# Kernel tuning notes

Measured on AMD Instinct MI355X. Metric: run time of the kernel, lower is better.

The kernel has to match this reference:

```python
import jax, jax.numpy as jnp
import numpy as np

B, IC2, N, K = 8, 128, 2048, 32   # x: [B, 2*in_channels, N, k]
C, G = 64, 8                       # out_channels, groups
CPG = C // G                       # channels per group
EPS_BN = 1e-5


def conv1x1(x, w, b=None):
    # 1x1 conv over [B, Cin, N, K] with weight [Cout, Cin]
    y = jnp.einsum('oc,bcnk->bonk', w, x)
    if b is not None:
        y = y + b[None, :, None, None]
    return y


def bn(x, g, beta, m, v):
    # inference-mode BatchNorm2d
    scale = g / jnp.sqrt(v + EPS_BN)
    return x * scale[None, :, None, None] + (beta - m * scale)[None, :, None, None]


def lrelu(x):
    return jax.nn.leaky_relu(x, 0.2)


def setup_inputs() -> dict:
    key = jax.random.key(0)
    ks = jax.random.split(key, 32)
    d = {}
    d['x'] = jax.random.normal(ks[0], (B, IC2, N, K), jnp.float32)
    d['rel_pos'] = jax.random.normal(ks[1], (B, 3, N, K), jnp.float32)
    # pos_net
    d['pos_w1'] = jax.random.normal(ks[2], (C, 3), jnp.float32) * 0.1
    d['pos_bn_g'] = jax.random.uniform(ks[3], (C,), jnp.float32, 0.5, 1.5)
    d['pos_bn_b'] = jax.random.normal(ks[4], (C,), jnp.float32) * 0.1
    d['pos_bn_m'] = jax.random.normal(ks[5], (C,), jnp.float32) * 0.1
    d['pos_bn_v'] = jax.random.uniform(ks[6], (C,), jnp.float32, 0.5, 1.5)
    d['pos_w2'] = jax.random.normal(ks[7], (C, C), jnp.float32) * 0.1
    d['pos_b2'] = jax.random.normal(ks[8], (C,), jnp.float32) * 0.1
    # pe_proj
    d['pe_w'] = jax.random.normal(ks[9], (G, C), jnp.float32) * 0.1
    d['pe_b'] = jax.random.normal(ks[10], (G,), jnp.float32) * 0.1
    # trans (Conv+BN+LeakyReLU)
    d['trans_w'] = jax.random.normal(ks[11], (C, IC2), jnp.float32) * 0.1
    d['trans_bn_g'] = jax.random.uniform(ks[12], (C,), jnp.float32, 0.5, 1.5)
    d['trans_bn_b'] = jax.random.normal(ks[13], (C,), jnp.float32) * 0.1
    d['trans_bn_m'] = jax.random.normal(ks[14], (C,), jnp.float32) * 0.1
    d['trans_bn_v'] = jax.random.uniform(ks[15], (C,), jnp.float32, 0.5, 1.5)
    # gate_net (hidden 16)
    d['gate_w1'] = jax.random.normal(ks[16], (16, IC2), jnp.float32) * 0.1
    d['gate_bn_g'] = jax.random.uniform(ks[17], (16,), jnp.float32, 0.5, 1.5)
    d['gate_bn_b'] = jax.random.normal(ks[18], (16,), jnp.float32) * 0.1
    d['gate_bn_m'] = jax.random.normal(ks[19], (16,), jnp.float32) * 0.1
    d['gate_bn_v'] = jax.random.uniform(ks[20], (16,), jnp.float32, 0.5, 1.5)
    d['gate_w2'] = jax.random.normal(ks[21], (1, 16), jnp.float32) * 0.1
    d['gate_b2'] = jnp.full((1,), 2.0, jnp.float32)  # init.constant_(bias, 2.0)
    # attn_net (hidden C//4 = 16)
    d['attn_w1'] = jax.random.normal(ks[22], (C // 4, IC2), jnp.float32) * 0.1
    d['attn_bn_g'] = jax.random.uniform(ks[23], (C // 4,), jnp.float32, 0.5, 1.5)
    d['attn_bn_b'] = jax.random.normal(ks[24], (C // 4,), jnp.float32) * 0.1
    d['attn_bn_m'] = jax.random.normal(ks[25], (C // 4,), jnp.float32) * 0.1
    d['attn_bn_v'] = jax.random.uniform(ks[26], (C // 4,), jnp.float32, 0.5, 1.5)
    d['attn_w2'] = jax.random.normal(ks[27], (G, C // 4), jnp.float32) * 0.1
    d['attn_b2'] = jax.random.normal(ks[28], (G,), jnp.float32) * 0.1
    return d


def reference(x, rel_pos, pos_w1, pos_bn_g, pos_bn_b, pos_bn_m, pos_bn_v, pos_w2, pos_b2,
              pe_w, pe_b, trans_w, trans_bn_g, trans_bn_b, trans_bn_m, trans_bn_v,
              gate_w1, gate_bn_g, gate_bn_b, gate_bn_m, gate_bn_v, gate_w2, gate_b2,
              attn_w1, attn_bn_g, attn_bn_b, attn_bn_m, attn_bn_v, attn_w2, attn_b2):
    # pos_net: conv -> BN -> LeakyReLU -> conv(bias)
    pos_enc = conv1x1(lrelu(bn(conv1x1(rel_pos, pos_w1), pos_bn_g, pos_bn_b, pos_bn_m, pos_bn_v)),
                      pos_w2, pos_b2)                                    # [B,C,N,K]
    # trans: conv -> BN -> LeakyReLU, plus positional encoding
    trans_feat = lrelu(bn(conv1x1(x, trans_w), trans_bn_g, trans_bn_b, trans_bn_m, trans_bn_v)) + pos_enc
    # gate_net (dropout=identity in eval): -> sigmoid gate [B,1,N,K]
    gate_h = lrelu(bn(conv1x1(x, gate_w1), gate_bn_g, gate_bn_b, gate_bn_m, gate_bn_v))
    gate_map = jax.nn.sigmoid(conv1x1(gate_h, gate_w2, gate_b2))
    # attn_net -> grouped logits [B,G,N,K]
    attn_h = lrelu(bn(conv1x1(x, attn_w1), attn_bn_g, attn_bn_b, attn_bn_m, attn_bn_v))
    attn_logits = conv1x1(attn_h, attn_w2, attn_b2)
    attn_logits = attn_logits + conv1x1(pos_enc, pe_w, pe_b)             # pe_proj
    attn_logits = attn_logits + jnp.log(gate_map + 1e-6)                 # full mode: log-combine gate
    attn_w = jax.nn.softmax(attn_logits, axis=-1)                        # softmax over neighbors k
    attn_w_exp = jnp.repeat(attn_w, CPG, axis=1)                         # repeat_interleave -> [B,C,N,K]
    out_attn = jnp.sum(trans_feat * attn_w_exp, axis=-1)                 # [B,C,N]
    out_max = jnp.max(trans_feat * gate_map, axis=-1)                    # [B,C,N]
    return out_attn + out_max
```

## Files before the change

kernel.cpp:

```cpp
#include <hip/hip_runtime.h>


typedef __attribute__((ext_vector_type(8))) short bf16x8;
typedef __attribute__((ext_vector_type(4))) float f32x4;

#define EPS_BN 1e-5f

__device__ __forceinline__ unsigned pk2(float a, float b){
  unsigned ua = __float_as_uint(a) + 0x8000u;
  unsigned ub = __float_as_uint(b) + 0x8000u;
  return __builtin_amdgcn_perm(ub, ua, 0x07060302);
}
__device__ __forceinline__ short f2bf(float a){
  unsigned u = __float_as_uint(a);
  u += 0x7FFFu + ((u >> 16) & 1u);
  return (short)(u >> 16);
}
__device__ __forceinline__ bf16x8 mk8(float4 a, float4 b){
  union { bf16x8 v; unsigned u[4]; } t;
  t.u[0] = pk2(a.x, a.y); t.u[1] = pk2(a.z, a.w);
  t.u[2] = pk2(b.x, b.y); t.u[3] = pk2(b.z, b.w);
  return t.v;
}
__device__ __forceinline__ float lrelu(float v){ return fmaxf(v, 0.2f*v); }

template<int N>
__device__ __forceinline__ float ror16(float x){
  return __int_as_float(__builtin_amdgcn_mov_dpp(__float_as_int(x), 0x120+N, 0xF, 0xF, false));
}
__device__ __forceinline__ float rsum16(float v){
  v += ror16<1>(v); v += ror16<2>(v); v += ror16<4>(v); v += ror16<8>(v); return v;
}
__device__ __forceinline__ float rmax16(float v){
  v = fmaxf(v, ror16<1>(v)); v = fmaxf(v, ror16<2>(v));
  v = fmaxf(v, ror16<4>(v)); v = fmaxf(v, ror16<8>(v)); return v;
}

#define MFMA16(a,b,c) __builtin_amdgcn_mfma_f32_16x16x32_bf16((a),(b),(c),0,0,0)

__global__ __launch_bounds__(256, 2)
void gsl_fused(const float* __restrict__ x,       const float* __restrict__ rel_pos,
               const float* __restrict__ pos_w1,  const float* __restrict__ pos_g,
               const float* __restrict__ pos_bb,  const float* __restrict__ pos_m,
               const float* __restrict__ pos_v,   const float* __restrict__ pos_w2,
               const float* __restrict__ pos_b2,  const float* __restrict__ pe_w,
               const float* __restrict__ pe_b,    const float* __restrict__ trans_w,
               const float* __restrict__ tr_g,    const float* __restrict__ tr_bb,
               const float* __restrict__ tr_m,    const float* __restrict__ tr_v,
               const float* __restrict__ gate_w1, const float* __restrict__ ga_g,
               const float* __restrict__ ga_bb,   const float* __restrict__ ga_m,
               const float* __restrict__ ga_v,    const float* __restrict__ gate_w2,
               const float* __restrict__ gate_b2, const float* __restrict__ attn_w1,
               const float* __restrict__ at_g,    const float* __restrict__ at_bb,
               const float* __restrict__ at_m,    const float* __restrict__ at_v,
               const float* __restrict__ attn_w2, const float* __restrict__ attn_b2,
               float* __restrict__ out)
{
  __shared__ __align__(16) char smem[73216];
  short* xbuf  = (short*)smem;
  short* wmain = (short*)(smem + 34816);
  short* wpos2 = (short*)(smem + 60928);
  float* trQ  = (float*)(smem + 71296);
  float* p1T  = (float*)(smem + 72320);
  float* gaT  = (float*)(smem + 72832);
  float* atT  = (float*)(smem + 72960);
  float* peBt = (float*)(smem + 73088);

  const int tid = threadIdx.x;
  const int wv  = tid >> 6;
  const int l   = tid & 63;
  const int l15 = l & 15, g4 = l >> 4;
  const int bid = blockIdx.x;
  const int b    = bid >> 6;
  const int nblk = (bid & 63) << 5;

  if (tid < 192){
    int r = tid >> 1, c0 = (tid & 1) * 64;
    const float* src = (r < 64) ? (trans_w + r*128)
                     : (r < 80) ? (gate_w1 + (r-64)*128)
                                : (attn_w1 + (r-80)*128);
    src += c0;
    short* dst = wmain + r*136 + c0;
    #pragma unroll
    for (int j = 0; j < 8; ++j)
      *(bf16x8*)(dst + 8*j) = mk8(*(const float4*)(src + 8*j), *(const float4*)(src + 8*j + 4));
  } else {
    int r = tid - 192;
    const float* src = pos_w2 + r*64;
    short* dst = wpos2 + r*72;
    #pragma unroll
    for (int j = 0; j < 8; ++j)
      *(bf16x8*)(dst + 8*j) = mk8(*(const float4*)(src + 8*j), *(const float4*)(src + 8*j + 4));
  }
  if (tid < 64){
    float s = tr_g[tid] * rsqrtf(tr_v[tid] + EPS_BN);
    *(float4*)(trQ + 4*tid) = make_float4(s, tr_bb[tid] - tr_m[tid]*s, pos_b2[tid], 0.f);
    float s2 = pos_g[tid] * rsqrtf(pos_v[tid] + EPS_BN);
    p1T[2*tid] = s2; p1T[2*tid+1] = pos_bb[tid] - pos_m[tid]*s2;
  } else if (tid < 80){
    int c = tid - 64;
    float s = ga_g[c] * rsqrtf(ga_v[c] + EPS_BN);
    gaT[2*c] = s; gaT[2*c+1] = ga_bb[c] - ga_m[c]*s;
  } else if (tid < 96){
    int c = tid - 80;
    float s = at_g[c] * rsqrtf(at_v[c] + EPS_BN);
    atT[2*c] = s; atT[2*c+1] = at_bb[c] - at_m[c]*s;
  } else if (tid < 112){
    int r2 = tid - 96;
    float v = 0.f;
    if (r2 < 8){
      v = pe_b[r2];
      for (int c = 0; c < 64; ++c) v += pe_w[r2*64 + c] * pos_b2[c];
    }
    peBt[r2] = v;
  }
  {
    int o = 2*tid, r = o >> 6, j = o & 63;
    float c0 = 0.f, c1 = 0.f;
    for (int c = 0; c < 64; ++c){
      float a = pe_w[r*64 + c];
      c0 += a * pos_w2[c*64 + j];
      c1 += a * pos_w2[c*64 + j + 1];
    }
    *(unsigned*)(wpos2 + (64 + r)*72 + j) = pk2(c0, c1);
  }

  uint2 pw1p[4];
  #pragma unroll
  for (int m2 = 0; m2 < 4; ++m2){
    uint2 t = make_uint2(0u, 0u);
    if (g4 == 0){
      const float* rp = pos_w1 + (16*m2 + l15)*3;
      t.x = pk2(rp[0], rp[1]);
      t.y = pk2(rp[2], 0.f);
    }
    pw1p[m2] = t;
  }
  bf16x8 gaf;
  {
    bf16x8 t = {0,0,0,0,0,0,0,0};
    #pragma unroll
    for (int j = 0; j < 8; ++j){
      int k = 8*g4 + j;
      float v2 = 0.f;
      if (l15 < 8)       { if (k >= 16) v2 = attn_w2[l15*16 + (k-16)]; }
      else if (l15 == 8) { if (k < 16)  v2 = gate_w2[k]; }
      t[j] = f2bf(v2);
    }
    gaf = t;
  }
  const float gb2v = gate_b2[0];

  __syncthreads();

  float lcr[4];
  #pragma unroll
  for (int r = 0; r < 4; ++r){
    int row = 4*g4 + r;
    lcr[r] = peBt[row] + ((row < 8) ? attn_b2[row] : 0.f);
  }

  const int col0 = 32*wv + l15, col1 = col0 + 16;
  const int lc0 = l15, lc1 = l15 + 16;
  const int lq = l & 7, ld = l >> 3;
  const int colb = 32*wv + 4*lq;
  char*  slice = smem + wv*8704;
  short* h1b   = (short*)slice;
  short* gab   = (short*)(slice + 4608);
  const float* xp0 = x + (((long)(b*128 + 8*ld)) << 16) + colb;
  const float* rpb = rel_pos + (((long)(3*b)) << 16);
  float* outb = out + (((long)(b*64)) << 11) + nblk + wv;

  f32x4 fa[8], fb[8];
  float rc[6] = {0.f,0.f,0.f,0.f,0.f,0.f};
  {
    const long sb0 = (long)nblk * 32;
    #pragma unroll
    for (int j = 0; j < 8; ++j) fa[j] = *(const f32x4*)(xp0 + sb0 + (((long)j) << 16));
    #pragma unroll
    for (int j = 0; j < 8; ++j) fb[j] = *(const f32x4*)(xp0 + sb0 + (((long)(64+j)) << 16));
    if (g4 == 0){
      long sg = sb0 + col0;
      rc[0] = rpb[sg];          rc[1] = rpb[sg + 65536];      rc[2] = rpb[sg + 131072];
      rc[3] = rpb[sg + 16];     rc[4] = rpb[sg + 65536 + 16]; rc[5] = rpb[sg + 131072 + 16];
    }
  }

  for (int it = 0; it < 8; ++it){
    const long sbase = (long)nblk*32 + 128*it;

    #pragma unroll
    for (int i2 = 0; i2 < 4; ++i2){
      union { bf16x8 v; unsigned u[4]; } ta, tb2;
      ta.u[0] = pk2(fa[0][i2], fa[1][i2]); ta.u[1] = pk2(fa[2][i2], fa[3][i2]);
      ta.u[2] = pk2(fa[4][i2], fa[5][i2]); ta.u[3] = pk2(fa[6][i2], fa[7][i2]);
      *(bf16x8*)(xbuf + (colb+i2)*136 + 8*ld) = ta.v;
      tb2.u[0] = pk2(fb[0][i2], fb[1][i2]); tb2.u[1] = pk2(fb[2][i2], fb[3][i2]);
      tb2.u[2] = pk2(fb[4][i2], fb[5][i2]); tb2.u[3] = pk2(fb[6][i2], fb[7][i2]);
      *(bf16x8*)(xbuf + (colb+i2)*136 + 64 + 8*ld) = tb2.v;
    }

    const long nsb = sbase + ((it < 7) ? 128 : 0);
    #pragma unroll
    for (int j = 0; j < 8; ++j) fa[j] = *(const f32x4*)(xp0 + nsb + (((long)j) << 16));

    f32x4 acc[6][2];
    #pragma unroll
    for (int m = 0; m < 6; ++m){
      f32x4 z = {0.f,0.f,0.f,0.f};
      acc[m][0] = z; acc[m][1] = z;
    }
    #pragma unroll
    for (int ks = 0; ks < 4; ++ks){
      bf16x8 b0 = *(const bf16x8*)(xbuf + col0*136 + 32*ks + 8*g4);
      bf16x8 b1 = *(const bf16x8*)(xbuf + col1*136 + 32*ks + 8*g4);
      #pragma unroll
      for (int m = 0; m < 6; ++m){
        bf16x8 af = *(const bf16x8*)(wmain + (16*m + l15)*136 + 32*ks + 8*g4);
        acc[m][0] = MFMA16(af, b0, acc[m][0]);
        acc[m][1] = MFMA16(af, b1, acc[m][1]);
      }
    }

    #pragma unroll
    for (int j = 0; j < 8; ++j) fb[j] = *(const f32x4*)(xp0 + nsb + (((long)(64+j)) << 16));

    {
      bf16x8 rf0 = {0,0,0,0,0,0,0,0}, rf1 = {0,0,0,0,0,0,0,0};
      if (g4 == 0){
        union { bf16x8 v; unsigned u[4]; } t0, t1;
        t0.u[0] = pk2(rc[0], rc[1]); t0.u[1] = pk2(rc[2], 0.f); t0.u[2] = 0u; t0.u[3] = 0u;
        t1.u[0] = pk2(rc[3], rc[4]); t1.u[1] = pk2(rc[5], 0.f); t1.u[2] = 0u; t1.u[3] = 0u;
        rf0 = t0.v; rf1 = t1.v;
      }
      #pragma unroll
      for (int m2 = 0; m2 < 4; ++m2){
        union { bf16x8 v; unsigned u[4]; } aw;
        aw.u[0] = pw1p[m2].x; aw.u[1] = pw1p[m2].y; aw.u[2] = 0u; aw.u[3] = 0u;
        f32x4 z = {0.f,0.f,0.f,0.f};
        f32x4 d0 = MFMA16(aw.v, rf0, z);
        f32x4 d1 = MFMA16(aw.v, rf1, z);
        int cb2 = 16*m2 + 4*g4;
        float2 t0 = *(const float2*)(p1T + 2*(cb2+0));
        float2 t1 = *(const float2*)(p1T + 2*(cb2+1));
        float2 t2 = *(const float2*)(p1T + 2*(cb2+2));
        float2 t3 = *(const float2*)(p1T + 2*(cb2+3));
        float h0 = lrelu(t0.x*d0[0]+t0.y), h1v = lrelu(t1.x*d0[1]+t1.y);
        float h2 = lrelu(t2.x*d0[2]+t2.y), h3 = lrelu(t3.x*d0[3]+t3.y);
        *(uint2*)(h1b + lc0*72 + cb2) = make_uint2(pk2(h0,h1v), pk2(h2,h3));
        h0 = lrelu(t0.x*d1[0]+t0.y); h1v = lrelu(t1.x*d1[1]+t1.y);
        h2 = lrelu(t2.x*d1[2]+t2.y); h3 = lrelu(t3.x*d1[3]+t3.y);
        *(uint2*)(h1b + lc1*72 + cb2) = make_uint2(pk2(h0,h1v), pk2(h2,h3));
      }
    }
    if (g4 == 0){
      long sg = nsb + col0;
      rc[0] = rpb[sg];          rc[1] = rpb[sg + 65536];      rc[2] = rpb[sg + 131072];
      rc[3] = rpb[sg + 16];     rc[4] = rpb[sg + 65536 + 16]; rc[5] = rpb[sg + 131072 + 16];
    }

    #pragma unroll
    for (int m = 0; m < 4; ++m)
      #pragma unroll
      for (int r = 0; r < 4; ++r){
        float4 tq = *(const float4*)(trQ + 4*(16*m + 4*g4 + r));
        acc[m][0][r] = lrelu(tq.x*acc[m][0][r] + tq.y) + tq.z;
        acc[m][1][r] = lrelu(tq.x*acc[m][1][r] + tq.y) + tq.z;
      }

    f32x4 pac4[2];
    {
      f32x4 z = {0.f,0.f,0.f,0.f};
      pac4[0] = z; pac4[1] = z;
    }
    #pragma unroll
    for (int ks = 0; ks < 2; ++ks){
      bf16x8 h0 = *(const bf16x8*)(h1b + lc0*72 + 32*ks + 8*g4);
      bf16x8 h1v = *(const bf16x8*)(h1b + lc1*72 + 32*ks + 8*g4);
      #pragma unroll
      for (int m2 = 0; m2 < 4; ++m2){
        bf16x8 af = *(const bf16x8*)(wpos2 + (16*m2 + l15)*72 + 32*ks + 8*g4);
        acc[m2][0] = MFMA16(af, h0, acc[m2][0]);
        acc[m2][1] = MFMA16(af, h1v, acc[m2][1]);
      }
      bf16x8 af4 = *(const bf16x8*)(wpos2 + (64 + l15)*72 + 32*ks + 8*g4);
      pac4[0] = MFMA16(af4, h0, pac4[0]);
      pac4[1] = MFMA16(af4, h1v, pac4[1]);
    }

    {
      int hc = 4*g4;
      float2 g0p = *(const float2*)(gaT + 2*(hc+0));
      float2 g1p = *(const float2*)(gaT + 2*(hc+1));
      float2 g2p = *(const float2*)(gaT + 2*(hc+2));
      float2 g3p = *(const float2*)(gaT + 2*(hc+3));
      float2 a0p = *(const float2*)(atT + 2*(hc+0));
      float2 a1p = *(const float2*)(atT + 2*(hc+1));
      float2 a2p = *(const float2*)(atT + 2*(hc+2));
      float2 a3p = *(const float2*)(atT + 2*(hc+3));
      #pragma unroll
      for (int ct = 0; ct < 2; ++ct){
        int lc = (ct == 0) ? lc0 : lc1;
        float q0 = lrelu(g0p.x*acc[4][ct][0] + g0p.y), q1 = lrelu(g1p.x*acc[4][ct][1] + g1p.y);
        float q2 = lrelu(g2p.x*acc[4][ct][2] + g2p.y), q3 = lrelu(g3p.x*acc[4][ct][3] + g3p.y);
        *(uint2*)(gab + lc*40 + hc) = make_uint2(pk2(q0,q1), pk2(q2,q3));
        float a0 = lrelu(a0p.x*acc[5][ct][0] + a0p.y), a1 = lrelu(a1p.x*acc[5][ct][1] + a1p.y);
        float a2 = lrelu(a2p.x*acc[5][ct][2] + a2p.y), a3 = lrelu(a3p.x*acc[5][ct][3] + a3p.y);
        *(uint2*)(gab + lc*40 + 16 + hc) = make_uint2(pk2(a0,a1), pk2(a2,a3));
      }
    }

    f32x4 gac0 = {0.f,0.f,0.f,0.f}, gac1 = gac0;
    {
      bf16x8 g0 = *(const bf16x8*)(gab + lc0*40 + 8*g4);
      bf16x8 g1 = *(const bf16x8*)(gab + lc1*40 + 8*g4);
      gac0 = MFMA16(gaf, g0, gac0);
      gac1 = MFMA16(gaf, g1, gac1);
    }

    float gv0 = __shfl(gac0[0], 32 + l15, 64);
    float gv1 = __shfl(gac1[0], 32 + l15, 64);
    float gm0 = 1.f/(1.f + __expf(-(gv0 + gb2v)));
    float gm1 = 1.f/(1.f + __expf(-(gv1 + gb2v)));
    float lg0 = __logf(gm0 + 1e-6f), lg1 = __logf(gm1 + 1e-6f);

    float wg0[4], wg1[4];
    #pragma unroll
    for (int r = 0; r < 4; ++r){
      float t0 = gac0[r] + pac4[0][r] + lcr[r] + lg0;
      float t1 = gac1[r] + pac4[1][r] + lcr[r] + lg1;
      float mx = rmax16(fmaxf(t0, t1));
      float e0 = __expf(t0 - mx), e1 = __expf(t1 - mx);
      float inv = 1.f / rsum16(e0 + e1);
      wg0[r] = e0 * inv; wg1[r] = e1 * inv;
    }
    float wf0[8], wf1[8];
    #pragma unroll
    for (int gg = 0; gg < 8; ++gg){
      int src = 16*(gg >> 2) + l15;
      wf0[gg] = __shfl(wg0[gg & 3], src, 64);
      wf1[gg] = __shfl(wg1[gg & 3], src, 64);
    }
    const bool hi = (g4 >= 2);
    #pragma unroll
    for (int m = 0; m < 4; ++m){
      float w0 = hi ? wf0[2*m+1] : wf0[2*m];
      float w1 = hi ? wf1[2*m+1] : wf1[2*m];
      #pragma unroll
      for (int r = 0; r < 4; ++r){
        float sA = rsum16(acc[m][0][r]*w0 + acc[m][1][r]*w1);
        float sM = rmax16(fmaxf(acc[m][0][r]*gm0, acc[m][1][r]*gm1));
        if (l15 == 0)
          outb[(((long)(16*m + 4*g4 + r)) << 11) + 4*it] = sA + sM;
      }
    }
  }
}

extern "C" void kernel_launch(void* const* d_in, const int* in_sizes, int n_in,
                              void* d_out, int out_size, void* d_ws, size_t ws_size,
                              hipStream_t stream){
  (void)in_sizes; (void)n_in; (void)out_size; (void)d_ws; (void)ws_size;
  gsl_fused<<<dim3(512), dim3(256), 0, stream>>>(
    (const float*)d_in[0],  (const float*)d_in[1],  (const float*)d_in[2],
    (const float*)d_in[3],  (const float*)d_in[4],  (const float*)d_in[5],
    (const float*)d_in[6],  (const float*)d_in[7],  (const float*)d_in[8],
    (const float*)d_in[9],  (const float*)d_in[10], (const float*)d_in[11],
    (const float*)d_in[12], (const float*)d_in[13], (const float*)d_in[14],
    (const float*)d_in[15], (const float*)d_in[16], (const float*)d_in[17],
    (const float*)d_in[18], (const float*)d_in[19], (const float*)d_in[20],
    (const float*)d_in[21], (const float*)d_in[22], (const float*)d_in[23],
    (const float*)d_in[24], (const float*)d_in[25], (const float*)d_in[26],
    (const float*)d_in[27], (const float*)d_in[28], (const float*)d_in[29],
    (float*)d_out);
}
```

Baseline: 75.63 us.

## Load x directly into MFMA fragments, drop LDS staging, split prep kernel

Each lane now loads x straight from global memory in the layout the MFMA B-operand needs and converts it to bf16 in registers. This removes the shared-memory x staging buffer, its write/read traffic and the associated bank pressure. The pe_w·pos_w2 fold and the pe bias are moved into a separate one-block prep kernel that writes to the workspace, which removes per-block redundant work. LDS shrinks and row padding changes, the grid doubles to 1024 blocks of 16 points each, and launch bounds target 3 blocks per SM. In exchange, the scalar strided global loads are less coalesced, register pressure rises, and there is an extra kernel launch.

```diff
diff --git a/kernel.cpp b/kernel.cpp
--- a/kernel.cpp
+++ b/kernel.cpp
@@ -16,13 +16,18 @@
   u += 0x7FFFu + ((u >> 16) & 1u);
   return (short)(u >> 16);
 }
-__device__ __forceinline__ bf16x8 mk8(float4 a, float4 b){
-  union { bf16x8 v; unsigned u[4]; } t;
-  t.u[0] = pk2(a.x, a.y); t.u[1] = pk2(a.z, a.w);
-  t.u[2] = pk2(b.x, b.y); t.u[3] = pk2(b.z, b.w);
-  return t.v;
-}
 __device__ __forceinline__ float lrelu(float v){ return fmaxf(v, 0.2f*v); }
+
+__device__ __forceinline__ void st8(short* dst, float4 a, float4 b){
+  *(uint2*)(dst)     = make_uint2(pk2(a.x,a.y), pk2(a.z,a.w));
+  *(uint2*)(dst + 4) = make_uint2(pk2(b.x,b.y), pk2(b.z,b.w));
+}
+__device__ __forceinline__ bf16x8 ld8(const short* p){
+  union { bf16x8 v; uint2 q[2]; } w;
+  w.q[0] = *(const uint2*)(p);
+  w.q[1] = *(const uint2*)(p + 4);
+  return w.v;
+}
 
 template<int N>
 __device__ __forceinline__ float ror16(float x){
@@ -38,13 +43,49 @@
 
 #define MFMA16(a,b,c) __builtin_amdgcn_mfma_f32_16x16x32_bf16((a),(b),(c),0,0,0)
 
-__global__ __launch_bounds__(256, 2)
+__device__ __forceinline__ void loadfrag(float (&t)[32], const float* xc, long sg){
+  #pragma unroll
+  for (int ks = 0; ks < 4; ++ks)
+    #pragma unroll
+    for (int j = 0; j < 8; ++j)
+      t[ks*8+j] = xc[(((long)(32*ks + j)) << 16) + sg];
+}
+__device__ __forceinline__ void cvtfrag(bf16x8 (&xb)[4], const float (&t)[32]){
+  #pragma unroll
+  for (int ks = 0; ks < 4; ++ks){
+    union { bf16x8 v; unsigned u[4]; } w;
+    w.u[0] = pk2(t[8*ks+0], t[8*ks+1]);
+    w.u[1] = pk2(t[8*ks+2], t[8*ks+3]);
+    w.u[2] = pk2(t[8*ks+4], t[8*ks+5]);
+    w.u[3] = pk2(t[8*ks+6], t[8*ks+7]);
+    xb[ks] = w.v;
+  }
+}
+
+__global__ void gsl_prep(const float* __restrict__ pos_w2, const float* __restrict__ pe_w,
+                         const float* __restrict__ pe_b,   const float* __restrict__ pos_b2,
+                         float* __restrict__ ws){
+  int t = threadIdx.x;
+  int r = t >> 6, j = t & 63;
+  float s = 0.f;
+  for (int c = 0; c < 64; ++c) s += pe_w[r*64 + c] * pos_w2[c*64 + j];
+  ws[t] = s;
+  if (t < 16){
+    float v = 0.f;
+    if (t < 8){
+      v = pe_b[t];
+      for (int c = 0; c < 64; ++c) v += pe_w[t*64 + c] * pos_b2[c];
+    }
+    ws[512 + t] = v;
+  }
+}
+
+__global__ __launch_bounds__(256, 3)
 void gsl_fused(const float* __restrict__ x,       const float* __restrict__ rel_pos,
                const float* __restrict__ pos_w1,  const float* __restrict__ pos_g,
                const float* __restrict__ pos_bb,  const float* __restrict__ pos_m,
                const float* __restrict__ pos_v,   const float* __restrict__ pos_w2,
-               const float* __restrict__ pos_b2,  const float* __restrict__ pe_w,
-               const float* __restrict__ pe_b,    const float* __restrict__ trans_w,
+               const float* __restrict__ pos_b2,  const float* __restrict__ trans_w,
                const float* __restrict__ tr_g,    const float* __restrict__ tr_bb,
                const float* __restrict__ tr_m,    const float* __restrict__ tr_v,
                const float* __restrict__ gate_w1, const float* __restrict__ ga_g,
@@ -54,25 +95,45 @@
                const float* __restrict__ at_g,    const float* __restrict__ at_bb,
                const float* __restrict__ at_m,    const float* __restrict__ at_v,
                const float* __restrict__ attn_w2, const float* __restrict__ attn_b2,
-               float* __restrict__ out)
+               const float* __restrict__ ws,      float* __restrict__ out)
 {
-  __shared__ __align__(16) char smem[73216];
-  short* xbuf  = (short*)smem;
-  short* wmain = (short*)(smem + 34816);
-  short* wpos2 = (short*)(smem + 60928);
-  float* trQ  = (float*)(smem + 71296);
-  float* p1T  = (float*)(smem + 72320);
-  float* gaT  = (float*)(smem + 72832);
-  float* atT  = (float*)(smem + 72960);
-  float* peBt = (float*)(smem + 73088);
+  __shared__ __align__(16) char smem[54080];
+  short* wmain = (short*)smem;
+  short* wpos2 = (short*)(smem + 25344);
+  float* trT  = (float*)(smem + 52544);
+  float* pb2T = (float*)(smem + 53056);
+  float* p1T  = (float*)(smem + 53312);
+  float* gaT  = (float*)(smem + 53824);
+  float* atT  = (float*)(smem + 53952);
 
   const int tid = threadIdx.x;
   const int wv  = tid >> 6;
   const int l   = tid & 63;
   const int l15 = l & 15, g4 = l >> 4;
   const int bid = blockIdx.x;
-  const int b    = bid >> 6;
-  const int nblk = (bid & 63) << 5;
+  const int b    = bid >> 7;
+  const int nblk = (bid & 127) << 4;
+
+  const int col0 = 32*wv + l15, col1 = col0 + 16;
+  const int lc0 = l15, lc1 = l15 + 16;
+  const float* xcg = x + (((long)(b*128 + 8*g4)) << 16);
+  const float* rpb = rel_pos + (((long)(3*b)) << 16);
+  float* outb = out + (((long)(b*64)) << 11) + nblk + wv;
+  short* h1b = (short*)(smem + 35136 + wv*4352);
+  short* gab = h1b;
+
+  float t0[32], t1[32];
+  float rc[6] = {0.f,0.f,0.f,0.f,0.f,0.f};
+  {
+    const long sb0 = (long)nblk * 32;
+    loadfrag(t0, xcg, sb0 + col0);
+    loadfrag(t1, xcg, sb0 + col0 + 16);
+    if (g4 == 0){
+      long sg = sb0 + col0;
+      rc[0] = rpb[sg];          rc[1] = rpb[sg + 65536];      rc[2] = rpb[sg + 131072];
+      rc[3] = rpb[sg + 16];     rc[4] = rpb[sg + 65536 + 16]; rc[5] = rpb[sg + 131072 + 16];
+    }
+  }
 
   if (tid < 192){
     int r = tid >> 1, c0 = (tid & 1) * 64;
@@ -80,21 +141,30 @@
                      : (r < 80) ? (gate_w1 + (r-64)*128)
                                 : (attn_w1 + (r-80)*128);
     src += c0;
-    short* dst = wmain + r*136 + c0;
+    short* dst = wmain + r*132 + c0;
     #pragma unroll
     for (int j = 0; j < 8; ++j)
-      *(bf16x8*)(dst + 8*j) = mk8(*(const float4*)(src + 8*j), *(const float4*)(src + 8*j + 4));
+      st8(dst + 8*j, *(const float4*)(src + 8*j), *(const float4*)(src + 8*j + 4));
   } else {
     int r = tid - 192;
     const float* src = pos_w2 + r*64;
-    short* dst = wpos2 + r*72;
+    short* dst = wpos2 + r*68;
     #pragma unroll
     for (int j = 0; j < 8; ++j)
-      *(bf16x8*)(dst + 8*j) = mk8(*(const float4*)(src + 8*j), *(const float4*)(src + 8*j + 4));
+      st8(dst + 8*j, *(const float4*)(src + 8*j), *(const float4*)(src + 8*j + 4));
+  }
+  if (tid < 16){
+    int r = tid >> 1, c0 = (tid & 1) * 32;
+    const float* src = ws + r*64 + c0;
+    short* dst = wpos2 + (64 + r)*68 + c0;
+    #pragma unroll
+    for (int j = 0; j < 4; ++j)
+      st8(dst + 8*j, *(const float4*)(src + 8*j), *(const float4*)(src + 8*j + 4));
   }
   if (tid < 64){
     float s = tr_g[tid] * rsqrtf(tr_v[tid] + EPS_BN);
-    *(float4*)(trQ + 4*tid) = make_float4(s, tr_bb[tid] - tr_m[tid]*s, pos_b2[tid], 0.f);
+    trT[2*tid] = s; trT[2*tid+1] = tr_bb[tid] - tr_m[tid]*s;
+    pb2T[tid] = pos_b2[tid];
     float s2 = pos_g[tid] * rsqrtf(pos_v[tid] + EPS_BN);
     p1T[2*tid] = s2; p1T[2*tid+1] = pos_bb[tid] - pos_m[tid]*s2;
   } else if (tid < 80){
@@ -105,24 +175,6 @@
     int c = tid - 80;
     float s = at_g[c] * rsqrtf(at_v[c] + EPS_BN);
     atT[2*c] = s; atT[2*c+1] = at_bb[c] - at_m[c]*s;
-  } else if (tid < 112){
-    int r2 = tid - 96;
-    float v = 0.f;
-    if (r2 < 8){
-      v = pe_b[r2];
-      for (int c = 0; c < 64; ++c) v += pe_w[r2*64 + c] * pos_b2[c];
-    }
-    peBt[r2] = v;
-  }
-  {
-    int o = 2*tid, r = o >> 6, j = o & 63;
-    float c0 = 0.f, c1 = 0.f;
-    for (int c = 0; c < 64; ++c){
-      float a = pe_w[r*64 + c];
-      c0 += a * pos_w2[c*64 + j];
-      c1 += a * pos_w2[c*64 + j + 1];
-    }
-    *(unsigned*)(wpos2 + (64 + r)*72 + j) = pk2(c0, c1);
   }
 
   uint2 pw1p[4];
@@ -150,59 +202,22 @@
     gaf = t;
   }
   const float gb2v = gate_b2[0];
-
-  __syncthreads();
-
   float lcr[4];
   #pragma unroll
   for (int r = 0; r < 4; ++r){
     int row = 4*g4 + r;
-    lcr[r] = peBt[row] + ((row < 8) ? attn_b2[row] : 0.f);
-  }
-
-  const int col0 = 32*wv + l15, col1 = col0 + 16;
-  const int lc0 = l15, lc1 = l15 + 16;
-  const int lq = l & 7, ld = l >> 3;
-  const int colb = 32*wv + 4*lq;
-  char*  slice = smem + wv*8704;
-  short* h1b   = (short*)slice;
-  short* gab   = (short*)(slice + 4608);
-  const float* xp0 = x + (((long)(b*128 + 8*ld)) << 16) + colb;
-  const float* rpb = rel_pos + (((long)(3*b)) << 16);
-  float* outb = out + (((long)(b*64)) << 11) + nblk + wv;
-
-  f32x4 fa[8], fb[8];
-  float rc[6] = {0.f,0.f,0.f,0.f,0.f,0.f};
-  {
-    const long sb0 = (long)nblk * 32;
-    #pragma unroll
-    for (int j = 0; j < 8; ++j) fa[j] = *(const f32x4*)(xp0 + sb0 + (((long)j) << 16));
-    #pragma unroll
-    for (int j = 0; j < 8; ++j) fb[j] = *(const f32x4*)(xp0 + sb0 + (((long)(64+j)) << 16));
-    if (g4 == 0){
-      long sg = sb0 + col0;
-      rc[0] = rpb[sg];          rc[1] = rpb[sg + 65536];      rc[2] = rpb[sg + 131072];
-      rc[3] = rpb[sg + 16];     rc[4] = rpb[sg + 65536 + 16]; rc[5] = rpb[sg + 131072 + 16];
-    }
-  }
-
-  for (int it = 0; it < 8; ++it){
+    lcr[r] = ws[512 + row] + ((row < 8) ? attn_b2[row] : 0.f);
+  }
+
+  bf16x8 xb0[4], xb1[4];
+  cvtfrag(xb0, t0);
+  cvtfrag(xb1, t1);
+
+  __syncthreads();
+
+  for (int it = 0; it < 4; ++it){
     const long sbase = (long)nblk*32 + 128*it;
-
-    #pragma unroll
-    for (int i2 = 0; i2 < 4; ++i2){
-      union { bf16x8 v; unsigned u[4]; } ta, tb2;
-      ta.u[0] = pk2(fa[0][i2], fa[1][i2]); ta.u[1] = pk2(fa[2][i2], fa[3][i2]);
-      ta.u[2] = pk2(fa[4][i2], fa[5][i2]); ta.u[3] = pk2(fa[6][i2], fa[7][i2]);
-      *(bf16x8*)(xbuf + (colb+i2)*136 + 8*ld) = ta.v;
-      tb2.u[0] = pk2(fb[0][i2], fb[1][i2]); tb2.u[1] = pk2(fb[2][i2], fb[3][i2]);
-      tb2.u[2] = pk2(fb[4][i2], fb[5][i2]); tb2.u[3] = pk2(fb[6][i2], fb[7][i2]);
-      *(bf16x8*)(xbuf + (colb+i2)*136 + 64 + 8*ld) = tb2.v;
-    }
-
-    const long nsb = sbase + ((it < 7) ? 128 : 0);
-    #pragma unroll
-    for (int j = 0; j < 8; ++j) fa[j] = *(const f32x4*)(xp0 + nsb + (((long)j) << 16));
+    const long nsb = sbase + ((it < 3) ? 128 : 0);
 
     f32x4 acc[6][2];
     #pragma unroll
@@ -212,26 +227,23 @@
     }
     #pragma unroll
     for (int ks = 0; ks < 4; ++ks){
-      bf16x8 b0 = *(const bf16x8*)(xbuf + col0*136 + 32*ks + 8*g4);
-      bf16x8 b1 = *(const bf16x8*)(xbuf + col1*136 + 32*ks + 8*g4);
       #pragma unroll
       for (int m = 0; m < 6; ++m){
-        bf16x8 af = *(const bf16x8*)(wmain + (16*m + l15)*136 + 32*ks + 8*g4);
-        acc[m][0] = MFMA16(af, b0, acc[m][0]);
-        acc[m][1] = MFMA16(af, b1, acc[m][1]);
-      }
-    }
-
-    #pragma unroll
-    for (int j = 0; j < 8; ++j) fb[j] = *(const f32x4*)(xp0 + nsb + (((long)(64+j)) << 16));
+        bf16x8 af = ld8(wmain + (16*m + l15)*132 + 32*ks + 8*g4);
+        acc[m][0] = MFMA16(af, xb0[ks], acc[m][0]);
+        acc[m][1] = MFMA16(af, xb1[ks], acc[m][1]);
+      }
+    }
+
+    loadfrag(t0, xcg, nsb + col0);
 
     {
       bf16x8 rf0 = {0,0,0,0,0,0,0,0}, rf1 = {0,0,0,0,0,0,0,0};
       if (g4 == 0){
-        union { bf16x8 v; unsigned u[4]; } t0, t1;
-        t0.u[0] = pk2(rc[0], rc[1]); t0.u[1] = pk2(rc[2], 0.f); t0.u[2] = 0u; t0.u[3] = 0u;
-        t1.u[0] = pk2(rc[3], rc[4]); t1.u[1] = pk2(rc[5], 0.f); t1.u[2] = 0u; t1.u[3] = 0u;
-        rf0 = t0.v; rf1 = t1.v;
+        union { bf16x8 v; unsigned u[4]; } q0, q1;
+        q0.u[0] = pk2(rc[0], rc[1]); q0.u[1] = pk2(rc[2], 0.f); q0.u[2] = 0u; q0.u[3] = 0u;
+        q1.u[0] = pk2(rc[3], rc[4]); q1.u[1] = pk2(rc[5], 0.f); q1.u[2] = 0u; q1.u[3] = 0u;
+        rf0 = q0.v; rf1 = q1.v;
       }
       #pragma unroll
       for (int m2 = 0; m2 < 4; ++m2){
@@ -241,16 +253,16 @@
         f32x4 d0 = MFMA16(aw.v, rf0, z);
         f32x4 d1 = MFMA16(aw.v, rf1, z);
         int cb2 = 16*m2 + 4*g4;
-        float2 t0 = *(const float2*)(p1T + 2*(cb2+0));
-        float2 t1 = *(const float2*)(p1T + 2*(cb2+1));
-        float2 t2 = *(const float2*)(p1T + 2*(cb2+2));
-        float2 t3 = *(const float2*)(p1T + 2*(cb2+3));
-        float h0 = lrelu(t0.x*d0[0]+t0.y), h1v = lrelu(t1.x*d0[1]+t1.y);
-        float h2 = lrelu(t2.x*d0[2]+t2.y), h3 = lrelu(t3.x*d0[3]+t3.y);
-        *(uint2*)(h1b + lc0*72 + cb2) = make_uint2(pk2(h0,h1v), pk2(h2,h3));
-        h0 = lrelu(t0.x*d1[0]+t0.y); h1v = lrelu(t1.x*d1[1]+t1.y);
-        h2 = lrelu(t2.x*d1[2]+t2.y); h3 = lrelu(t3.x*d1[3]+t3.y);
-        *(uint2*)(h1b + lc1*72 + cb2) = make_uint2(pk2(h0,h1v), pk2(h2,h3));
+        float2 q0 = *(const float2*)(p1T + 2*(cb2+0));
+        float2 q1 = *(const float2*)(p1T + 2*(cb2+1));
+        float2 q2 = *(const float2*)(p1T + 2*(cb2+2));
+        float2 q3 = *(const float2*)(p1T + 2*(cb2+3));
+        float h0 = lrelu(q0.x*d0[0]+q0.y), h1v = lrelu(q1.x*d0[1]+q1.y);
+        float h2 = lrelu(q2.x*d0[2]+q2.y), h3 = lrelu(q3.x*d0[3]+q3.y);
+        *(uint2*)(h1b + lc0*68 + cb2) = make_uint2(pk2(h0,h1v), pk2(h2,h3));
+        h0 = lrelu(q0.x*d1[0]+q0.y); h1v = lrelu(q1.x*d1[1]+q1.y);
+        h2 = lrelu(q2.x*d1[2]+q2.y); h3 = lrelu(q3.x*d1[3]+q3.y);
+        *(uint2*)(h1b + lc1*68 + cb2) = make_uint2(pk2(h0,h1v), pk2(h2,h3));
       }
     }
     if (g4 == 0){
@@ -260,13 +272,18 @@
     }
 
     #pragma unroll
-    for (int m = 0; m < 4; ++m)
-      #pragma unroll
-      for (int r = 0; r < 4; ++r){
-        float4 tq = *(const float4*)(trQ + 4*(16*m + 4*g4 + r));
-        acc[m][0][r] = lrelu(tq.x*acc[m][0][r] + tq.y) + tq.z;
-        acc[m][1][r] = lrelu(tq.x*acc[m][1][r] + tq.y) + tq.z;
-      }
+    for (int m = 0; m < 4; ++m){
+      float4 tb01 = *(const float4*)(trT + 2*(16*m + 4*g4));
+      float4 tb23 = *(const float4*)(trT + 2*(16*m + 4*g4) + 4);
+      float4 pz   = *(const float4*)(pb2T + 16*m + 4*g4);
+      #pragma unroll
+      for (int ct = 0; ct < 2; ++ct){
+        acc[m][ct][0] = lrelu(tb01.x*acc[m][ct][0] + tb01.y) + pz.x;
+        acc[m][ct][1] = lrelu(tb01.z*acc[m][ct][1] + tb01.w) + pz.y;
+        acc[m][ct][2] = lrelu(tb23.x*acc[m][ct][2] + tb23.y) + pz.z;
+        acc[m][ct][3] = lrelu(tb23.z*acc[m][ct][3] + tb23.w) + pz.w;
+      }
+    }
 
     f32x4 pac4[2];
     {
@@ -275,18 +292,21 @@
     }
     #pragma unroll
     for (int ks = 0; ks < 2; ++ks){
-      bf16x8 h0 = *(const bf16x8*)(h1b + lc0*72 + 32*ks + 8*g4);
-      bf16x8 h1v = *(const bf16x8*)(h1b + lc1*72 + 32*ks + 8*g4);
+      bf16x8 h0 = ld8(h1b + lc0*68 + 32*ks + 8*g4);
+      bf16x8 h1v = ld8(h1b + lc1*68 + 32*ks + 8*g4);
       #pragma unroll
       for (int m2 = 0; m2 < 4; ++m2){
-        bf16x8 af = *(const bf16x8*)(wpos2 + (16*m2 + l15)*72 + 32*ks + 8*g4);
+        bf16x8 af = ld8(wpos2 + (16*m2 + l15)*68 + 32*ks + 8*g4);
         acc[m2][0] = MFMA16(af, h0, acc[m2][0]);
         acc[m2][1] = MFMA16(af, h1v, acc[m2][1]);
       }
-      bf16x8 af4 = *(const bf16x8*)(wpos2 + (64 + l15)*72 + 32*ks + 8*g4);
+      bf16x8 af4 = ld8(wpos2 + (64 + l15)*68 + 32*ks + 8*g4);
       pac4[0] = MFMA16(af4, h0, pac4[0]);
       pac4[1] = MFMA16(af4, h1v, pac4[1]);
     }
+
+    cvtfrag(xb0, t0);
+    loadfrag(t1, xcg, nsb + col0 + 16);
 
     {
       int hc = 4*g4;
@@ -327,25 +347,23 @@
     float wg0[4], wg1[4];
     #pragma unroll
     for (int r = 0; r < 4; ++r){
-      float t0 = gac0[r] + pac4[0][r] + lcr[r] + lg0;
-      float t1 = gac1[r] + pac4[1][r] + lcr[r] + lg1;
-      float mx = rmax16(fmaxf(t0, t1));
-      float e0 = __expf(t0 - mx), e1 = __expf(t1 - mx);
+      float tt0 = gac0[r] + pac4[0][r] + lcr[r] + lg0;
+      float tt1 = gac1[r] + pac4[1][r] + lcr[r] + lg1;
+      float mx = rmax16(fmaxf(tt0, tt1));
+      float e0 = __expf(tt0 - mx), e1 = __expf(tt1 - mx);
       float inv = 1.f / rsum16(e0 + e1);
       wg0[r] = e0 * inv; wg1[r] = e1 * inv;
     }
-    float wf0[8], wf1[8];
-    #pragma unroll
-    for (int gg = 0; gg < 8; ++gg){
-      int src = 16*(gg >> 2) + l15;
-      wf0[gg] = __shfl(wg0[gg & 3], src, 64);
-      wf1[gg] = __shfl(wg1[gg & 3], src, 64);
-    }
     const bool hi = (g4 >= 2);
     #pragma unroll
     for (int m = 0; m < 4; ++m){
-      float w0 = hi ? wf0[2*m+1] : wf0[2*m];
-      float w1 = hi ? wf1[2*m+1] : wf1[2*m];
+      int src = 16*(m >> 1) + l15;
+      float a0 = __shfl(wg0[(2*m) & 3], src, 64);
+      float b0 = __shfl(wg0[(2*m+1) & 3], src, 64);
+      float a1 = __shfl(wg1[(2*m) & 3], src, 64);
+      float b1 = __shfl(wg1[(2*m+1) & 3], src, 64);
+      float w0 = hi ? b0 : a0;
+      float w1 = hi ? b1 : a1;
       #pragma unroll
       for (int r = 0; r < 4; ++r){
         float sA = rsum16(acc[m][0][r]*w0 + acc[m][1][r]*w1);
@@ -354,23 +372,27 @@
           outb[(((long)(16*m + 4*g4 + r)) << 11) + 4*it] = sA + sM;
       }
     }
+
+    cvtfrag(xb1, t1);
   }
 }
 
 extern "C" void kernel_launch(void* const* d_in, const int* in_sizes, int n_in,
                               void* d_out, int out_size, void* d_ws, size_t ws_size,
                               hipStream_t stream){
-  (void)in_sizes; (void)n_in; (void)out_size; (void)d_ws; (void)ws_size;
-  gsl_fused<<<dim3(512), dim3(256), 0, stream>>>(
+  (void)in_sizes; (void)n_in; (void)out_size; (void)ws_size;
+  gsl_prep<<<dim3(1), dim3(512), 0, stream>>>(
+    (const float*)d_in[7], (const float*)d_in[9], (const float*)d_in[10],
+    (const float*)d_in[8], (float*)d_ws);
+  gsl_fused<<<dim3(1024), dim3(256), 0, stream>>>(
     (const float*)d_in[0],  (const float*)d_in[1],  (const float*)d_in[2],
     (const float*)d_in[3],  (const float*)d_in[4],  (const float*)d_in[5],
     (const float*)d_in[6],  (const float*)d_in[7],  (const float*)d_in[8],
-    (const float*)d_in[9],  (const float*)d_in[10], (const float*)d_in[11],
-    (const float*)d_in[12], (const float*)d_in[13], (const float*)d_in[14],
-    (const float*)d_in[15], (const float*)d_in[16], (const float*)d_in[17],
-    (const float*)d_in[18], (const float*)d_in[19], (const float*)d_in[20],
-    (const float*)d_in[21], (const float*)d_in[22], (const float*)d_in[23],
-    (const float*)d_in[24], (const float*)d_in[25], (const float*)d_in[26],
-    (const float*)d_in[27], (const float*)d_in[28], (const float*)d_in[29],
-    (float*)d_out);
-}
+    (const float*)d_in[11], (const float*)d_in[12], (const float*)d_in[13],
+    (const float*)d_in[14], (const float*)d_in[15], (const float*)d_in[16],
+    (const float*)d_in[17], (const float*)d_in[18], (const float*)d_in[19],
+    (const float*)d_in[20], (const float*)d_in[21], (const float*)d_in[22],
+    (const float*)d_in[23], (const float*)d_in[24], (const float*)d_in[25],
+    (const float*)d_in[26], (const float*)d_in[27], (const float*)d_in[28],
+    (const float*)d_in[29], (const float*)d_ws, (float*)d_out);
+}
```

After: 218.6 us. 2.89x slower.
